# Optimization experiments

Hardware: AMD Instinct MI355X
Metric: run time of the kernel (lower is better)

## Reference

```python
import jax, jax.numpy as jnp
import numpy as np

B, L, D_MODEL = 2, 2048, 1024
N_HEAD, D_K, D_V = 16, 64, 64


def setup_inputs() -> dict:
    key = jax.random.key(0)
    ks = jax.random.split(key, 11)
    s = lambda fan_in: 1.0 / np.sqrt(fan_in)
    return {
        "q": jax.random.normal(ks[0], (B, L, D_MODEL), dtype=jnp.float32),
        "k": jax.random.normal(ks[1], (B, L, D_MODEL), dtype=jnp.float32),
        "v": jax.random.normal(ks[2], (B, L, D_MODEL), dtype=jnp.float32),
        "Wq": jax.random.uniform(ks[3], (D_MODEL, N_HEAD * D_K), jnp.float32, -s(D_MODEL), s(D_MODEL)),
        "bq": jax.random.uniform(ks[4], (N_HEAD * D_K,), jnp.float32, -s(D_MODEL), s(D_MODEL)),
        "Wk": jax.random.uniform(ks[5], (D_MODEL, N_HEAD * D_K), jnp.float32, -s(D_MODEL), s(D_MODEL)),
        "bk": jax.random.uniform(ks[6], (N_HEAD * D_K,), jnp.float32, -s(D_MODEL), s(D_MODEL)),
        "Wv": jax.random.uniform(ks[7], (D_MODEL, N_HEAD * D_V), jnp.float32, -s(D_MODEL), s(D_MODEL)),
        "bv": jax.random.uniform(ks[8], (N_HEAD * D_V,), jnp.float32, -s(D_MODEL), s(D_MODEL)),
        "Wo": jax.random.uniform(ks[9], (N_HEAD * D_V, D_MODEL), jnp.float32, -s(N_HEAD * D_V), s(N_HEAD * D_V)),
        "bo": jax.random.uniform(ks[10], (D_MODEL,), jnp.float32, -s(N_HEAD * D_V), s(N_HEAD * D_V)),
    }


def reference(q, k, v, Wq, bq, Wk, bk, Wv, bv, Wo, bo):
    b, lq, _ = q.shape
    lk = k.shape[1]
    # QKV projections then split heads: [B, H, L, Dk]
    qh = (q @ Wq + bq).reshape(b, lq, N_HEAD, D_K).transpose(0, 2, 1, 3)
    kh = (k @ Wk + bk).reshape(b, lk, N_HEAD, D_K).transpose(0, 2, 1, 3)
    vh = (v @ Wv + bv).reshape(b, lk, N_HEAD, D_V).transpose(0, 2, 1, 3)
    # naive SDPA: materialize [B, H, Lq, Lk] scores, scale by sqrt(d_k)
    scores = jnp.einsum("bhqd,bhkd->bhqk", qh, kh) / jnp.sqrt(jnp.float32(D_K))
    attn = jax.nn.softmax(scores, axis=-1)
    out = jnp.einsum("bhqk,bhkd->bhqd", attn, vh)
    # merge heads and output projection (dropout = identity in eval)
    out = out.transpose(0, 2, 1, 3).reshape(b, lq, N_HEAD * D_V)
    out = out @ Wo + bo
    return out, attn
```

## Files before the change

kernel.cpp:

```cpp
#include <hip/hip_runtime.h>
#include <hip/hip_bf16.h>

typedef float f32x4 __attribute__((ext_vector_type(4)));
typedef short bf16x8 __attribute__((ext_vector_type(8)));

#define MFMA_BF16 __builtin_amdgcn_mfma_f32_16x16x32_bf16

static __device__ __forceinline__ unsigned short f2bf(float f) {
    __hip_bfloat16 h = __float2bfloat16(f);
    return __builtin_bit_cast(unsigned short, h);
}
static __device__ __forceinline__ unsigned int pack2(float a, float b) {
    return (unsigned int)f2bf(a) | ((unsigned int)f2bf(b) << 16);
}

static __device__ __forceinline__ void gl16(const unsigned short* g, unsigned short* l) {
    unsigned short* gg = const_cast<unsigned short*>(g);
    __builtin_amdgcn_global_load_lds(
        (__attribute__((address_space(1))) unsigned int*)gg,
        (__attribute__((address_space(3))) unsigned int*)l, 16, 0, 0);
}

__global__ __launch_bounds__(256) void conv_wT(
    const float* __restrict__ Wq, const float* __restrict__ Wk,
    const float* __restrict__ Wv, const float* __restrict__ Wo,
    unsigned short* __restrict__ WT)
{
    const int z = blockIdx.z;
    const float* W = (z == 0) ? Wq : (z == 1) ? Wk : (z == 2) ? Wv : Wo;
    unsigned short* Wt = WT + (size_t)z * 1048576;
    const int k0 = blockIdx.x * 64, n0 = blockIdx.y * 64;
    __shared__ float tl[64][68];
    const int t = threadIdx.x;
    const int r = t >> 2, cs = (t & 3) * 16;
#pragma unroll
    for (int j = 0; j < 4; j++)
        *(float4*)&tl[r][cs + j * 4] = *(const float4*)&W[(size_t)(k0 + r) * 1024 + n0 + cs + j * 4];
    __syncthreads();
    const int n = t & 63, kb = (t >> 6) * 16;
#pragma unroll
    for (int j = 0; j < 4; j++) {
        const int kk = kb + j * 4;
        uint2 o = { pack2(tl[kk][n], tl[kk + 1][n]), pack2(tl[kk + 2][n], tl[kk + 3][n]) };
        *(uint2*)&Wt[(size_t)(n0 + n) * 1024 + k0 + kk] = o;
    }
}

__global__ __launch_bounds__(256) void conv_bf16(
    const float* __restrict__ q, const float* __restrict__ k, const float* __restrict__ v,
    unsigned short* __restrict__ qkvb)
{
    const int z = blockIdx.y;
    const float* s = (z == 0) ? q : (z == 1) ? k : v;
    unsigned short* d = qkvb + (size_t)z * 4194304;
    const size_t i = ((size_t)blockIdx.x * 256 + threadIdx.x) * 8;
    float4 a = *(const float4*)&s[i], b = *(const float4*)&s[i + 4];
    uint4 o = { pack2(a.x, a.y), pack2(a.z, a.w), pack2(b.x, b.y), pack2(b.z, b.w) };
    *(uint4*)&d[i] = o;
}

static __device__ __forceinline__ void gemm_core(
    const unsigned short* __restrict__ A, const unsigned short* __restrict__ Bt,
    unsigned short* lA, unsigned short* lB, int m0, int n0, f32x4 (&acc)[4][4])
{
    const int t = threadIdx.x;
    const int w = t >> 6, lane = t & 63, lrow = lane & 15, lkg = lane >> 4;
    const int wr = w >> 1, wc = w & 1;
    const int srow = lane >> 2, sseg = (lane & 3) * 8;

    const unsigned short* Ab0 = &A[(size_t)(m0 + w * 32 + srow) * 1024 + sseg];
    const unsigned short* Ab1 = &A[(size_t)(m0 + w * 32 + 16 + srow) * 1024 + sseg];
    const unsigned short* Bb0 = &Bt[(size_t)(n0 + w * 32 + srow) * 1024 + sseg];
    const unsigned short* Bb1 = &Bt[(size_t)(n0 + w * 32 + 16 + srow) * 1024 + sseg];

#define GISSUE(tt, buf)                                     \
    do {                                                    \
        const int k0_ = (tt) * 32;                          \
        gl16(Ab0 + k0_, &lA[(buf) * 4096 + w * 1024]);      \
        gl16(Ab1 + k0_, &lA[(buf) * 4096 + w * 1024 + 512]);\
        gl16(Bb0 + k0_, &lB[(buf) * 4096 + w * 1024]);      \
        gl16(Bb1 + k0_, &lB[(buf) * 4096 + w * 1024 + 512]);\
    } while (0)

    GISSUE(0, 0);
    GISSUE(1, 1);
    __builtin_amdgcn_sched_barrier(0);

    int bcur = 0;
    for (int tt = 0; tt < 32; ++tt) {
        if (tt < 31) { asm volatile("s_waitcnt vmcnt(4)"); }
        else         { asm volatile("s_waitcnt vmcnt(0)"); }
        __builtin_amdgcn_s_barrier();
        __builtin_amdgcn_sched_barrier(0);
        if (tt + 2 < 32) {
            int bpre = bcur + 2; if (bpre >= 3) bpre -= 3;
            GISSUE(tt + 2, bpre);
        }
        __builtin_amdgcn_sched_barrier(0);

        const unsigned short* la = &lA[bcur * 4096];
        const unsigned short* lb = &lB[bcur * 4096];
        bf16x8 af[4], bfr[4];
#pragma unroll
        for (int mi = 0; mi < 4; mi++)
            af[mi] = *(const bf16x8*)&la[(wr * 64 + mi * 16 + lrow) * 32 + lkg * 8];
#pragma unroll
        for (int ni = 0; ni < 4; ni++)
            bfr[ni] = *(const bf16x8*)&lb[(wc * 64 + ni * 16 + lrow) * 32 + lkg * 8];
        __builtin_amdgcn_s_setprio(1);
#pragma unroll
        for (int mi = 0; mi < 4; mi++)
#pragma unroll
            for (int ni = 0; ni < 4; ni++)
                acc[mi][ni] = MFMA_BF16(af[mi], bfr[ni], acc[mi][ni], 0, 0, 0);
        __builtin_amdgcn_s_setprio(0);
        bcur = (bcur == 2) ? 0 : bcur + 1;
    }
#undef GISSUE
}

__global__ __launch_bounds__(256) void gemm_qkv(
    const unsigned short* __restrict__ qkvb, const unsigned short* __restrict__ WT,
    const float* __restrict__ bq, const float* __restrict__ bk, const float* __restrict__ bv,
    unsigned short* __restrict__ Qh, unsigned short* __restrict__ Kh, unsigned short* __restrict__ Vt)
{
    const int u0 = blockIdx.x;
    const int u = (u0 & 7) * 96 + (u0 >> 3);
    const int z = u >> 8, rm = u & 255;
    const int m0 = ((rm >> 3) & 31) * 128, n0 = (rm & 7) * 128;

    const unsigned short* A = qkvb + (size_t)z * 4194304;
    const unsigned short* Bt = WT + (size_t)z * 1048576;
    const float* bias = (z == 0) ? bq : (z == 1) ? bk : bv;

    __shared__ unsigned short lA[3 * 4096], lB[3 * 4096];
    f32x4 acc[4][4];
#pragma unroll
    for (int i = 0; i < 4; i++)
#pragma unroll
        for (int j = 0; j < 4; j++) acc[i][j] = (f32x4){0.f, 0.f, 0.f, 0.f};

    gemm_core(A, Bt, lA, lB, m0, n0, acc);

    const int t = threadIdx.x;
    const int w = t >> 6, lane = t & 63, lrow = lane & 15, lkg = lane >> 4;
    const int wr = w >> 1, wc = w & 1;

#pragma unroll
    for (int mi = 0; mi < 4; mi++) {
#pragma unroll
        for (int ni = 0; ni < 4; ni++) {
            const int gn = n0 + wc * 64 + ni * 16 + lrow;
            const float bb = bias[gn];
            const int hh = gn >> 6, dk = gn & 63;
            const int gm0 = m0 + wr * 64 + mi * 16 + lkg * 4;
            const int b2 = gm0 >> 11, ll = gm0 & 2047;
            if (z < 2) {
                unsigned short* C = (z == 0) ? Qh : Kh;
#pragma unroll
                for (int r = 0; r < 4; r++)
                    C[(size_t)((b2 * 16 + hh) * 2048 + ll + r) * 64 + dk] = f2bf(acc[mi][ni][r] + bb);
            } else {
                uint2 o = { pack2(acc[mi][ni][0] + bb, acc[mi][ni][1] + bb),
                            pack2(acc[mi][ni][2] + bb, acc[mi][ni][3] + bb) };
                *(uint2*)&Vt[(size_t)((b2 * 16 + hh) * 64 + dk) * 2048 + ll] = o;
            }
        }
    }
}

__global__ __launch_bounds__(256) void gemm_o(
    const unsigned short* __restrict__ Oh, const unsigned short* __restrict__ WoT,
    const float* __restrict__ bo, float* __restrict__ out)
{
    const int u0 = blockIdx.x;
    const int u = (u0 & 7) * 32 + (u0 >> 3);
    const int m0 = (u >> 3) * 128, n0 = (u & 7) * 128;

    __shared__ unsigned short lA[3 * 4096], lB[3 * 4096];
    f32x4 acc[4][4];
#pragma unroll
    for (int i = 0; i < 4; i++)
#pragma unroll
        for (int j = 0; j < 4; j++) acc[i][j] = (f32x4){0.f, 0.f, 0.f, 0.f};

    gemm_core(Oh, WoT, lA, lB, m0, n0, acc);

    const int t = threadIdx.x;
    const int w = t >> 6, lane = t & 63, lrow = lane & 15, lkg = lane >> 4;
    const int wr = w >> 1, wc = w & 1;

#pragma unroll
    for (int mi = 0; mi < 4; mi++) {
#pragma unroll
        for (int ni = 0; ni < 4; ni++) {
            const int gn = n0 + wc * 64 + ni * 16 + lrow;
            const float bb = bo[gn];
            const int gm0 = m0 + wr * 64 + mi * 16 + lkg * 4;
#pragma unroll
            for (int r = 0; r < 4; r++)
                out[(size_t)(gm0 + r) * 1024 + gn] = acc[mi][ni][r] + bb;
        }
    }
}

__global__ __launch_bounds__(512, 4) void attn_kernel(
    const unsigned short* __restrict__ Qh, const unsigned short* __restrict__ Kh,
    const unsigned short* __restrict__ Vt, float* __restrict__ attn,
    unsigned short* __restrict__ Oh)
{
    const int bid = blockIdx.x;
    const int swz = (bid & 7) * 64 + (bid >> 3);
    const int bh = swz >> 4;
    const int q0 = (swz & 15) * 128;
    const int b = bh >> 4, h = bh & 15;
    const int t = threadIdx.x;
    const int w = t >> 6, lane = t & 63, ql = lane & 15, kg = lane >> 4;

    __shared__ unsigned short lS[2][8192];
    __shared__ float stg[8][1024];

    const size_t kvbase = (size_t)bh * 2048 * 64;
    const float C = 0.18033688011112042f;

    const unsigned short* qptr = Qh + kvbase + (size_t)(q0 + w * 16 + ql) * 64 + kg * 8;
    const bf16x8 qf0 = *(const bf16x8*)(qptr);
    const bf16x8 qf1 = *(const bf16x8*)(qptr + 32);

    const unsigned short* Kbh = Kh + kvbase;
    const unsigned short* Vbh = Vt + kvbase;

    const int kr = w * 8 + (lane >> 3);
    const int kc = (lane & 7) ^ (kr & 7);
    const int r7 = ql & 7;

    f32x4 ls4 = (f32x4){0.f, 0.f, 0.f, 0.f};
    {
        gl16(Kbh + (size_t)kr * 64 + kc * 8, &lS[0][w * 512]);
        gl16(Kbh + (size_t)(kr + 64) * 64 + kc * 8, &lS[0][4096 + w * 512]);
        __syncthreads();
        for (int kt = 0; kt < 16; ++kt) {
            const int c = kt & 1;
            if (kt < 15) {
                const int k0n = (kt + 1) * 128;
                gl16(Kbh + (size_t)(k0n + kr) * 64 + kc * 8, &lS[c ^ 1][w * 512]);
                gl16(Kbh + (size_t)(k0n + kr + 64) * 64 + kc * 8, &lS[c ^ 1][4096 + w * 512]);
            } else {
                gl16(Kbh + (size_t)kr * 64 + kc * 8, &lS[0][w * 512]);
                gl16(Vbh + (size_t)kr * 2048 + kc * 8, &lS[0][4096 + w * 512]);
            }
            const unsigned short* Kl = lS[c];
            f32x4 sacc[8];
            __builtin_amdgcn_s_setprio(1);
#pragma unroll
            for (int ni = 0; ni < 8; ni++) {
                const int rb = (ni * 16 + ql) * 64;
                bf16x8 kf0 = *(const bf16x8*)&Kl[rb + ((kg ^ r7) * 8)];
                bf16x8 kf1 = *(const bf16x8*)&Kl[rb + (((4 + kg) ^ r7) * 8)];
                f32x4 s = (f32x4){0.f, 0.f, 0.f, 0.f};
                s = MFMA_BF16(kf0, qf0, s, 0, 0, 0);
                sacc[ni] = MFMA_BF16(kf1, qf1, s, 0, 0, 0);
            }
            __builtin_amdgcn_s_setprio(0);
#pragma unroll
            for (int ni = 0; ni < 8; ni++)
#pragma unroll
                for (int r = 0; r < 4; r++) ls4[r] += exp2f(sacc[ni][r] * C);
            __syncthreads();
        }
    }
    float lsum = ls4[0] + ls4[1] + ls4[2] + ls4[3];
    lsum += __shfl_xor(lsum, 16);
    lsum += __shfl_xor(lsum, 32);
    const float mlg = -log2f(lsum);

    f32x4 acco[4];
#pragma unroll
    for (int nv = 0; nv < 4; nv++) acco[nv] = (f32x4){0.f, 0.f, 0.f, 0.f};

    float* abase = attn + ((size_t)bh * 2048 + q0 + w * 16) * 2048 + ql * 4;

    for (int kt = 0; kt < 32; ++kt) {
        const int c = kt & 1;
        if (kt < 31) {
            const int k0n = (kt + 1) * 64;
            gl16(Kbh + (size_t)(k0n + kr) * 64 + kc * 8, &lS[c ^ 1][w * 512]);
            gl16(Vbh + (size_t)kr * 2048 + k0n + kc * 8, &lS[c ^ 1][4096 + w * 512]);
        }
        __builtin_amdgcn_sched_barrier(0);
        const int k0 = kt * 64;
        const unsigned short* Kl = lS[c];
        const unsigned short* Vl = &lS[c][4096];

        f32x4 sacc[4];
        __builtin_amdgcn_s_setprio(1);
#pragma unroll
        for (int ni = 0; ni < 4; ni++) {
            const int rb = (ni * 16 + ql) * 64;
            bf16x8 kf0 = *(const bf16x8*)&Kl[rb + ((kg ^ r7) * 8)];
            bf16x8 kf1 = *(const bf16x8*)&Kl[rb + (((4 + kg) ^ r7) * 8)];
            f32x4 s = (f32x4){0.f, 0.f, 0.f, 0.f};
            s = MFMA_BF16(kf0, qf0, s, 0, 0, 0);
            sacc[ni] = MFMA_BF16(kf1, qf1, s, 0, 0, 0);
        }
        __builtin_amdgcn_s_setprio(0);

#pragma unroll
        for (int ni = 0; ni < 4; ni++) {
            f32x4 p;
#pragma unroll
            for (int r = 0; r < 4; r++) p[r] = exp2f(fmaf(sacc[ni][r], C, mlg));
            *(f32x4*)&stg[w][ql * 64 + ni * 16 + kg * 4] = p;
        }

#pragma unroll
        for (int i = 0; i < 4; i++) {
            const int row = i * 4 + kg;
            f32x4 vv = *(const f32x4*)&stg[w][row * 64 + ql * 4];
            __builtin_nontemporal_store(vv, (f32x4*)&abase[(size_t)row * 2048 + k0]);
        }

        __builtin_amdgcn_s_setprio(1);
#pragma unroll
        for (int s4 = 0; s4 < 2; s4++) {
            const float* ps = &stg[w][ql * 64 + s4 * 32 + kg * 8];
            f32x4 pa = *(const f32x4*)ps;
            f32x4 pb = *(const f32x4*)(ps + 4);
            uint4 pw = { pack2(pa[0], pa[1]), pack2(pa[2], pa[3]),
                         pack2(pb[0], pb[1]), pack2(pb[2], pb[3]) };
            bf16x8 pf = __builtin_bit_cast(bf16x8, pw);
#pragma unroll
            for (int nv = 0; nv < 4; nv++) {
                const int cc = (s4 * 4 + kg) ^ r7;
                bf16x8 vf = *(const bf16x8*)&Vl[(nv * 16 + ql) * 64 + cc * 8];
                acco[nv] = MFMA_BF16(vf, pf, acco[nv], 0, 0, 0);
            }
        }
        __builtin_amdgcn_s_setprio(0);

        asm volatile("s_waitcnt vmcnt(4)");
        __builtin_amdgcn_s_barrier();
        __builtin_amdgcn_sched_barrier(0);
    }
    asm volatile("s_waitcnt vmcnt(0)");

    unsigned short* obase = Oh + ((size_t)(b * 2048 + q0 + w * 16 + ql)) * 1024 + h * 64 + kg * 4;
#pragma unroll
    for (int nv = 0; nv < 4; nv++) {
        uint2 o2 = { pack2(acco[nv][0], acco[nv][1]), pack2(acco[nv][2], acco[nv][3]) };
        *(uint2*)&obase[nv * 16] = o2;
    }
}

extern "C" void kernel_launch(void* const* d_in, const int* in_sizes, int n_in,
                              void* d_out, int out_size, void* d_ws, size_t ws_size,
                              hipStream_t stream) {
    const float* q  = (const float*)d_in[0];
    const float* k  = (const float*)d_in[1];
    const float* v  = (const float*)d_in[2];
    const float* Wq = (const float*)d_in[3];
    const float* bq = (const float*)d_in[4];
    const float* Wk = (const float*)d_in[5];
    const float* bk = (const float*)d_in[6];
    const float* Wv = (const float*)d_in[7];
    const float* bv = (const float*)d_in[8];
    const float* Wo = (const float*)d_in[9];
    const float* bo = (const float*)d_in[10];

    float* out  = (float*)d_out;
    float* attn = out + (size_t)2 * 2048 * 1024;

    const size_t HS = 4194304;
    unsigned short* qkvb = (unsigned short*)d_ws;
    unsigned short* WT   = qkvb + 3 * HS;
    unsigned short* Qh   = WT + 4 * 1048576;
    unsigned short* Kh   = Qh + HS;
    unsigned short* Vt   = Kh + HS;
    unsigned short* Oh   = Vt + HS;

    conv_wT  <<<dim3(16, 16, 4), 256, 0, stream>>>(Wq, Wk, Wv, Wo, WT);
    conv_bf16<<<dim3(2048, 3),  256, 0, stream>>>(q, k, v, qkvb);
    gemm_qkv <<<dim3(768), 256, 0, stream>>>(qkvb, WT, bq, bk, bv, Qh, Kh, Vt);
    attn_kernel<<<dim3(512), 512, 0, stream>>>(Qh, Kh, Vt, attn, Oh);
    gemm_o   <<<dim3(256), 256, 0, stream>>>(Oh, WT + 3 * 1048576, bo, out);
}
```

Before: 242.3 us.

## Shrink attention blocks to 64 queries and reuse LDS for staging

The attention kernel now runs 1024 blocks of 256 threads, each covering 64 query rows instead of 128, and LDS use drops from 64KB to 32KB. The probability staging buffer aliases the first-pass K double buffer. The second pass uses a single K/V buffer that is refilled after a barrier, and the attn row stores are issued after that load. The goal is more resident blocks per CU and better overlap of the global attn writes with the loads. The cost is that K is streamed twice as often overall and the second pass loses its double buffering.

```diff
diff --git a/kernel.cpp b/kernel.cpp
--- a/kernel.cpp
+++ b/kernel.cpp
@@ -204,21 +204,21 @@
     }
 }
 
-__global__ __launch_bounds__(512, 4) void attn_kernel(
+__global__ __launch_bounds__(256, 4) void attn_kernel(
     const unsigned short* __restrict__ Qh, const unsigned short* __restrict__ Kh,
     const unsigned short* __restrict__ Vt, float* __restrict__ attn,
     unsigned short* __restrict__ Oh)
 {
     const int bid = blockIdx.x;
-    const int swz = (bid & 7) * 64 + (bid >> 3);
-    const int bh = swz >> 4;
-    const int q0 = (swz & 15) * 128;
+    const int swz = (bid & 7) * 128 + (bid >> 3);
+    const int bh = swz >> 5;
+    const int q0 = (swz & 31) * 64;
     const int b = bh >> 4, h = bh & 15;
     const int t = threadIdx.x;
     const int w = t >> 6, lane = t & 63, ql = lane & 15, kg = lane >> 4;
 
-    __shared__ unsigned short lS[2][8192];
-    __shared__ float stg[8][1024];
+    __shared__ unsigned short regA[8192];
+    __shared__ unsigned short kv[8192];
 
     const size_t kvbase = (size_t)bh * 2048 * 64;
     const float C = 0.18033688011112042f;
@@ -230,30 +230,32 @@
     const unsigned short* Kbh = Kh + kvbase;
     const unsigned short* Vbh = Vt + kvbase;
 
-    const int kr = w * 8 + (lane >> 3);
+    const int kr = w * 16 + (lane >> 3);
     const int kc = (lane & 7) ^ (kr & 7);
     const int r7 = ql & 7;
 
     f32x4 ls4 = (f32x4){0.f, 0.f, 0.f, 0.f};
     {
-        gl16(Kbh + (size_t)kr * 64 + kc * 8, &lS[0][w * 512]);
-        gl16(Kbh + (size_t)(kr + 64) * 64 + kc * 8, &lS[0][4096 + w * 512]);
+        gl16(Kbh + (size_t)kr * 64 + kc * 8, &regA[w * 1024]);
+        gl16(Kbh + (size_t)(kr + 8) * 64 + kc * 8, &regA[w * 1024 + 512]);
         __syncthreads();
-        for (int kt = 0; kt < 16; ++kt) {
+        for (int kt = 0; kt < 32; ++kt) {
             const int c = kt & 1;
-            if (kt < 15) {
-                const int k0n = (kt + 1) * 128;
-                gl16(Kbh + (size_t)(k0n + kr) * 64 + kc * 8, &lS[c ^ 1][w * 512]);
-                gl16(Kbh + (size_t)(k0n + kr + 64) * 64 + kc * 8, &lS[c ^ 1][4096 + w * 512]);
+            if (kt < 31) {
+                const int k0n = (kt + 1) * 64;
+                gl16(Kbh + (size_t)(k0n + kr) * 64 + kc * 8, &regA[(c ^ 1) * 4096 + w * 1024]);
+                gl16(Kbh + (size_t)(k0n + kr + 8) * 64 + kc * 8, &regA[(c ^ 1) * 4096 + w * 1024 + 512]);
             } else {
-                gl16(Kbh + (size_t)kr * 64 + kc * 8, &lS[0][w * 512]);
-                gl16(Vbh + (size_t)kr * 2048 + kc * 8, &lS[0][4096 + w * 512]);
+                gl16(Kbh + (size_t)kr * 64 + kc * 8, &kv[w * 1024]);
+                gl16(Kbh + (size_t)(kr + 8) * 64 + kc * 8, &kv[w * 1024 + 512]);
+                gl16(Vbh + (size_t)kr * 2048 + kc * 8, &kv[4096 + w * 1024]);
+                gl16(Vbh + (size_t)(kr + 8) * 2048 + kc * 8, &kv[4096 + w * 1024 + 512]);
             }
-            const unsigned short* Kl = lS[c];
-            f32x4 sacc[8];
+            const unsigned short* Kl = &regA[c * 4096];
+            f32x4 sacc[4];
             __builtin_amdgcn_s_setprio(1);
 #pragma unroll
-            for (int ni = 0; ni < 8; ni++) {
+            for (int ni = 0; ni < 4; ni++) {
                 const int rb = (ni * 16 + ql) * 64;
                 bf16x8 kf0 = *(const bf16x8*)&Kl[rb + ((kg ^ r7) * 8)];
                 bf16x8 kf1 = *(const bf16x8*)&Kl[rb + (((4 + kg) ^ r7) * 8)];
@@ -263,7 +265,7 @@
             }
             __builtin_amdgcn_s_setprio(0);
 #pragma unroll
-            for (int ni = 0; ni < 8; ni++)
+            for (int ni = 0; ni < 4; ni++)
 #pragma unroll
                 for (int r = 0; r < 4; r++) ls4[r] += exp2f(sacc[ni][r] * C);
             __syncthreads();
@@ -278,27 +280,21 @@
 #pragma unroll
     for (int nv = 0; nv < 4; nv++) acco[nv] = (f32x4){0.f, 0.f, 0.f, 0.f};
 
+    float* stgW = (float*)regA + w * 1024;
+    const unsigned short* kvK = kv;
+    const unsigned short* kvV = kv + 4096;
     float* abase = attn + ((size_t)bh * 2048 + q0 + w * 16) * 2048 + ql * 4;
 
     for (int kt = 0; kt < 32; ++kt) {
-        const int c = kt & 1;
-        if (kt < 31) {
-            const int k0n = (kt + 1) * 64;
-            gl16(Kbh + (size_t)(k0n + kr) * 64 + kc * 8, &lS[c ^ 1][w * 512]);
-            gl16(Vbh + (size_t)kr * 2048 + k0n + kc * 8, &lS[c ^ 1][4096 + w * 512]);
-        }
-        __builtin_amdgcn_sched_barrier(0);
         const int k0 = kt * 64;
-        const unsigned short* Kl = lS[c];
-        const unsigned short* Vl = &lS[c][4096];
 
         f32x4 sacc[4];
         __builtin_amdgcn_s_setprio(1);
 #pragma unroll
         for (int ni = 0; ni < 4; ni++) {
             const int rb = (ni * 16 + ql) * 64;
-            bf16x8 kf0 = *(const bf16x8*)&Kl[rb + ((kg ^ r7) * 8)];
-            bf16x8 kf1 = *(const bf16x8*)&Kl[rb + (((4 + kg) ^ r7) * 8)];
+            bf16x8 kf0 = *(const bf16x8*)&kvK[rb + ((kg ^ r7) * 8)];
+            bf16x8 kf1 = *(const bf16x8*)&kvK[rb + (((4 + kg) ^ r7) * 8)];
             f32x4 s = (f32x4){0.f, 0.f, 0.f, 0.f};
             s = MFMA_BF16(kf0, qf0, s, 0, 0, 0);
             sacc[ni] = MFMA_BF16(kf1, qf1, s, 0, 0, 0);
@@ -310,20 +306,13 @@
             f32x4 p;
 #pragma unroll
             for (int r = 0; r < 4; r++) p[r] = exp2f(fmaf(sacc[ni][r], C, mlg));
-            *(f32x4*)&stg[w][ql * 64 + ni * 16 + kg * 4] = p;
-        }
-
-#pragma unroll
-        for (int i = 0; i < 4; i++) {
-            const int row = i * 4 + kg;
-            f32x4 vv = *(const f32x4*)&stg[w][row * 64 + ql * 4];
-            __builtin_nontemporal_store(vv, (f32x4*)&abase[(size_t)row * 2048 + k0]);
+            *(f32x4*)&stgW[ql * 64 + ni * 16 + kg * 4] = p;
         }
 
         __builtin_amdgcn_s_setprio(1);
 #pragma unroll
         for (int s4 = 0; s4 < 2; s4++) {
-            const float* ps = &stg[w][ql * 64 + s4 * 32 + kg * 8];
+            const float* ps = &stgW[ql * 64 + s4 * 32 + kg * 8];
             f32x4 pa = *(const f32x4*)ps;
             f32x4 pb = *(const f32x4*)(ps + 4);
             uint4 pw = { pack2(pa[0], pa[1]), pack2(pa[2], pa[3]),
@@ -332,11 +321,30 @@
 #pragma unroll
             for (int nv = 0; nv < 4; nv++) {
                 const int cc = (s4 * 4 + kg) ^ r7;
-                bf16x8 vf = *(const bf16x8*)&Vl[(nv * 16 + ql) * 64 + cc * 8];
+                bf16x8 vf = *(const bf16x8*)&kvV[(nv * 16 + ql) * 64 + cc * 8];
                 acco[nv] = MFMA_BF16(vf, pf, acco[nv], 0, 0, 0);
             }
         }
         __builtin_amdgcn_s_setprio(0);
+
+        __builtin_amdgcn_s_barrier();
+        __builtin_amdgcn_sched_barrier(0);
+
+        if (kt < 31) {
+            const int k0n = (kt + 1) * 64;
+            gl16(Kbh + (size_t)(k0n + kr) * 64 + kc * 8, &kv[w * 1024]);
+            gl16(Kbh + (size_t)(k0n + kr + 8) * 64 + kc * 8, &kv[w * 1024 + 512]);
+            gl16(Vbh + (size_t)kr * 2048 + k0n + kc * 8, &kv[4096 + w * 1024]);
+            gl16(Vbh + (size_t)(kr + 8) * 2048 + k0n + kc * 8, &kv[4096 + w * 1024 + 512]);
+        }
+        __builtin_amdgcn_sched_barrier(0);
+
+#pragma unroll
+        for (int i = 0; i < 4; i++) {
+            const int row = i * 4 + kg;
+            f32x4 vv = *(const f32x4*)&stgW[row * 64 + ql * 4];
+            __builtin_nontemporal_store(vv, (f32x4*)&abase[(size_t)row * 2048 + k0]);
+        }
 
         asm volatile("s_waitcnt vmcnt(4)");
         __builtin_amdgcn_s_barrier();
@@ -381,6 +389,6 @@
     conv_wT  <<<dim3(16, 16, 4), 256, 0, stream>>>(Wq, Wk, Wv, Wo, WT);
     conv_bf16<<<dim3(2048, 3),  256, 0, stream>>>(q, k, v, qkvb);
     gemm_qkv <<<dim3(768), 256, 0, stream>>>(qkvb, WT, bq, bk, bv, Qh, Kh, Vt);
-    attn_kernel<<<dim3(512), 512, 0, stream>>>(Qh, Kh, Vt, attn, Oh);
+    attn_kernel<<<dim3(1024), 256, 0, stream>>>(Qh, Kh, Vt, attn, Oh);
     gemm_o   <<<dim3(256), 256, 0, stream>>>(Oh, WT + 3 * 1048576, bo, out);
 }
```

New measurement: 242.2 us. No clear change (-0.1%).
